# Performance work log

Measured on AMD Instinct MI355X. Metric: run time of the kernel, lower is better.

Reference implementation:

```python
import jax, jax.numpy as jnp
import numpy as np

T, S, B, E, H, F = 100, 4096, 32, 256, 8, 2048
DH = E // H
EPS = 1e-5

def setup_inputs() -> dict:
    key = jax.random.key(0)
    ks = jax.random.split(key, 32)
    n = lambda i, shape, s=1.0: jax.random.normal(ks[i], shape, jnp.float32) * s
    inp = {
        'hidden_states': n(0, (T, B, E)),
        'query_pos': n(1, (T, B, E)),
        'enc_hidden': n(2, (S, B, E)),
        'enc_pos': n(3, (S, B, E)),
        'attn_mask': n(4, (B * H, T, S)),
        # cross-attn (nn.MultiheadAttention) params
        'ca_wq': n(5, (E, E), 0.02), 'ca_bq': jnp.zeros(E),
        'ca_wk': n(6, (E, E), 0.02), 'ca_bk': jnp.zeros(E),
        'ca_wv': n(7, (E, E), 0.02), 'ca_bv': jnp.zeros(E),
        'ca_wo': n(8, (E, E), 0.02), 'ca_bo': jnp.zeros(E),
        # self-attn (Mask2FormerAttention) params
        'sa_wq': n(9, (E, E), 0.02), 'sa_bq': jnp.zeros(E),
        'sa_wk': n(10, (E, E), 0.02), 'sa_bk': jnp.zeros(E),
        'sa_wv': n(11, (E, E), 0.02), 'sa_bv': jnp.zeros(E),
        'sa_wo': n(12, (E, E), 0.02), 'sa_bo': jnp.zeros(E),
        # layer norms
        'ln1_g': jnp.ones(E), 'ln1_b': jnp.zeros(E),
        'ln2_g': jnp.ones(E), 'ln2_b': jnp.zeros(E),
        'ln3_g': jnp.ones(E), 'ln3_b': jnp.zeros(E),
        # FFN
        'fc1_w': n(13, (F, E), 0.02), 'fc1_b': jnp.zeros(F),
        'fc2_w': n(14, (E, F), 0.02), 'fc2_b': jnp.zeros(E),
    }
    return inp

def _ln(x, g, b):
    m = jnp.mean(x, -1, keepdims=True)
    v = jnp.mean(jnp.square(x - m), -1, keepdims=True)
    return (x - m) * jax.lax.rsqrt(v + EPS) * g + b

def _mha(q_in, k_in, v_in, wq, bq, wk, bk, wv, bv, wo, bo, mask):
    # q_in: [B,T,E], k_in/v_in: [B,S,E], mask: [B*H,T,S] additive or None
    b, t, _ = q_in.shape
    s = k_in.shape[1]
    q = (q_in @ wq.T + bq) * (DH ** -0.5)
    k = k_in @ wk.T + bk
    v = v_in @ wv.T + bv
    q = q.reshape(b, t, H, DH).transpose(0, 2, 1, 3)  # [B,H,T,dh]
    k = k.reshape(b, s, H, DH).transpose(0, 2, 1, 3)
    v = v.reshape(b, s, H, DH).transpose(0, 2, 1, 3)
    scores = jnp.einsum('bhtd,bhsd->bhts', q, k)
    if mask is not None:
        scores = scores + mask.reshape(b, H, t, s)
    p = jax.nn.softmax(scores, axis=-1)
    o = jnp.einsum('bhts,bhsd->bhtd', p, v)
    o = o.transpose(0, 2, 1, 3).reshape(b, t, E)
    return o @ wo.T + bo

def reference(hidden_states, query_pos, enc_hidden, enc_pos, attn_mask,
              ca_wq, ca_bq, ca_wk, ca_bk, ca_wv, ca_bv, ca_wo, ca_bo,
              sa_wq, sa_bq, sa_wk, sa_bk, sa_wv, sa_bv, sa_wo, sa_bo,
              ln1_g, ln1_b, ln2_g, ln2_b, ln3_g, ln3_b,
              fc1_w, fc1_b, fc2_w, fc2_b):
    # convert seq-first [T,B,E] -> batch-first [B,T,E]
    hs = hidden_states.transpose(1, 0, 2)
    qp = query_pos.transpose(1, 0, 2)
    enc = enc_hidden.transpose(1, 0, 2)
    ep = enc_pos.transpose(1, 0, 2)
    # masked cross-attention (post-norm), dropout=0
    residual = hs
    x = _mha(hs + qp, enc + ep, enc,
             ca_wq, ca_bq, ca_wk, ca_bk, ca_wv, ca_bv, ca_wo, ca_bo, attn_mask)
    hs = _ln(residual + x, ln1_g, ln1_b)
    # self-attention with query pos embeddings on q and k, no mask
    residual = hs
    x = _mha(hs + qp, hs + qp, hs,
             sa_wq, sa_bq, sa_wk, sa_bk, sa_wv, sa_bv, sa_wo, sa_bo, None)
    hs = _ln(residual + x, ln2_g, ln2_b)
    # FFN
    x = jax.nn.relu(hs @ fc1_w.T + fc1_b) @ fc2_w.T + fc2_b
    hs = _ln(hs + x, ln3_g, ln3_b)
    return hs.transpose(1, 0, 2)  # back to [T,B,E]
```

## Files before the change

### kernel.cpp

```cpp
#include <hip/hip_runtime.h>
#include <hip/hip_bf16.h>
#include <math.h>

#define TQ 100
#define SS 4096
#define BB 32
#define EE 256
#define HH 8
#define FF 2048
#define DHH 32
#define LNEPS 1e-5f

typedef __attribute__((ext_vector_type(8))) short bf16x8;
typedef __attribute__((ext_vector_type(4))) short bf16x4;
typedef __attribute__((ext_vector_type(4))) float f32x4;

__device__ inline unsigned short f2bfu(float f) {
    __hip_bfloat16 h = __float2bfloat16(f);
    return *reinterpret_cast<unsigned short*>(&h);
}

#define PBM 64
#define PBK 32
#define PLDP 40
#define TLP 268

__global__ __launch_bounds__(256)
void cvt_all(const float* s0, const float* s1, const float* s2, const float* s3,
             const float* s4, const float* s5, const float* s6, const float* s7,
             const float* s8, const float* s9,
             unsigned short* d0, unsigned short* d1, unsigned short* d2, unsigned short* d3,
             unsigned short* d4, unsigned short* d5, unsigned short* d6, unsigned short* d7,
             unsigned short* d8, unsigned short* d9)
{
    const int bi = blockIdx.x;
    const float* s; unsigned short* d; int base;
    if (bi < 512) {
        const int seg = bi >> 6;
        base = (bi & 63) * 1024;
        switch (seg) {
            case 0: s = s0; d = d0; break;
            case 1: s = s1; d = d1; break;
            case 2: s = s2; d = d2; break;
            case 3: s = s3; d = d3; break;
            case 4: s = s4; d = d4; break;
            case 5: s = s5; d = d5; break;
            case 6: s = s6; d = d6; break;
            default: s = s7; d = d7; break;
        }
    } else {
        const int r = bi - 512;
        base = (r & 511) * 1024;
        if (r >> 9) { s = s9; d = d9; } else { s = s8; d = d8; }
    }
    const int i = base + threadIdx.x * 4;
    float4 v = *(const float4*)(s + i);
    ushort4 ov;
    ov.x = f2bfu(v.x); ov.y = f2bfu(v.y); ov.z = f2bfu(v.z); ov.w = f2bfu(v.w);
    *(ushort4*)(d + i) = ov;
}

__global__ __launch_bounds__(256)
void proj_kv(const float* __restrict__ enc, const float* __restrict__ ep,
             const __hip_bfloat16* __restrict__ Wk, const float* __restrict__ bk,
             const __hip_bfloat16* __restrict__ Wv, const float* __restrict__ bv,
             __hip_bfloat16* __restrict__ Kout, __hip_bfloat16* __restrict__ Vtout)
{
    __shared__ short Akv[PBM][PLDP];
    __shared__ short Av[PBM][PLDP];
    __shared__ short BkRaw[256 * PLDP];
    __shared__ short BvRaw[256 * PLDP];
    short (*Bk)[PLDP] = (short(*)[PLDP])BkRaw;
    short (*Bv)[PLDP] = (short(*)[PLDP])BvRaw;
    short (*tk)[TLP] = (short(*)[TLP])BkRaw;
    short (*tv)[TLP] = (short(*)[TLP])BvRaw;

    const int tid = threadIdx.x;
    const int m0 = blockIdx.x * PBM;
    const int b = m0 >> 12;
    const int s0 = m0 & (SS - 1);
    const int rr = tid >> 2;
    const int rc = (tid & 3) << 3;
    const long long abase = ((long long)(s0 + rr) * BB + b) * EE + rc;

    const int wv = tid >> 6, l = tid & 63;
    const int wm0 = (wv & 1) * 32, wn0 = (wv >> 1) * 128;
    const int lr16 = l & 15, lk8 = (l >> 4) * 8;

    f32x4 acck[2][8] = {};
    f32x4 accv[2][8] = {};

    for (int k0 = 0; k0 < EE; k0 += PBK) {
        float4 a0 = *(const float4*)(enc + abase + k0);
        float4 a1 = *(const float4*)(enc + abase + k0 + 4);
        float4 e0 = *(const float4*)(ep + abase + k0);
        float4 e1 = *(const float4*)(ep + abase + k0 + 4);
        bf16x8 pv, pkv;
        pv[0] = (short)f2bfu(a0.x); pv[1] = (short)f2bfu(a0.y);
        pv[2] = (short)f2bfu(a0.z); pv[3] = (short)f2bfu(a0.w);
        pv[4] = (short)f2bfu(a1.x); pv[5] = (short)f2bfu(a1.y);
        pv[6] = (short)f2bfu(a1.z); pv[7] = (short)f2bfu(a1.w);
        pkv[0] = (short)f2bfu(a0.x + e0.x); pkv[1] = (short)f2bfu(a0.y + e0.y);
        pkv[2] = (short)f2bfu(a0.z + e0.z); pkv[3] = (short)f2bfu(a0.w + e0.w);
        pkv[4] = (short)f2bfu(a1.x + e1.x); pkv[5] = (short)f2bfu(a1.y + e1.y);
        pkv[6] = (short)f2bfu(a1.z + e1.z); pkv[7] = (short)f2bfu(a1.w + e1.w);

        bf16x8 wkr[4], wvr[4];
        #pragma unroll
        for (int it = 0; it < 4; ++it) {
            wkr[it] = *(const bf16x8*)(Wk + (long long)(rr + it * 64) * EE + k0 + rc);
            wvr[it] = *(const bf16x8*)(Wv + (long long)(rr + it * 64) * EE + k0 + rc);
        }

        __syncthreads();
        *(bf16x8*)&Akv[rr][rc] = pkv;
        *(bf16x8*)&Av[rr][rc]  = pv;
        #pragma unroll
        for (int it = 0; it < 4; ++it) {
            *(bf16x8*)&Bk[rr + it * 64][rc] = wkr[it];
            *(bf16x8*)&Bv[rr + it * 64][rc] = wvr[it];
        }
        __syncthreads();

        bf16x8 ak0 = *(const bf16x8*)&Akv[wm0 + lr16][lk8];
        bf16x8 ak1 = *(const bf16x8*)&Akv[wm0 + 16 + lr16][lk8];
        bf16x8 av0 = *(const bf16x8*)&Av[wm0 + lr16][lk8];
        bf16x8 av1 = *(const bf16x8*)&Av[wm0 + 16 + lr16][lk8];
        #pragma unroll
        for (int j = 0; j < 8; ++j) {
            bf16x8 bk8 = *(const bf16x8*)&Bk[wn0 + j * 16 + lr16][lk8];
            bf16x8 bv8 = *(const bf16x8*)&Bv[wn0 + j * 16 + lr16][lk8];
            acck[0][j] = __builtin_amdgcn_mfma_f32_16x16x32_bf16(ak0, bk8, acck[0][j], 0, 0, 0);
            acck[1][j] = __builtin_amdgcn_mfma_f32_16x16x32_bf16(ak1, bk8, acck[1][j], 0, 0, 0);
            accv[0][j] = __builtin_amdgcn_mfma_f32_16x16x32_bf16(av0, bv8, accv[0][j], 0, 0, 0);
            accv[1][j] = __builtin_amdgcn_mfma_f32_16x16x32_bf16(av1, bv8, accv[1][j], 0, 0, 0);
        }
    }

    const int q4 = (l >> 4) * 4;
    #pragma unroll
    for (int h = 0; h < 2; ++h) {
        __syncthreads();
        if (wm0 == h * 32) {
            #pragma unroll
            for (int i = 0; i < 2; ++i) {
                #pragma unroll
                for (int j = 0; j < 8; ++j) {
                    const int n = wn0 + j * 16 + lr16;
                    const float bik = bk[n], biv = bv[n];
                    #pragma unroll
                    for (int r = 0; r < 4; ++r) {
                        tk[i * 16 + q4 + r][n] = (short)f2bfu(acck[i][j][r] + bik);
                        tv[i * 16 + q4 + r][n] = (short)f2bfu(accv[i][j][r] + biv);
                    }
                }
            }
        }
        __syncthreads();
        #pragma unroll
        for (int it = 0; it < 8; ++it) {
            const int r2 = wv * 8 + it;
            ushort4 v = *(const ushort4*)&tk[r2][l * 4];
            *(ushort4*)(Kout + (long long)(m0 + h * 32 + r2) * EE + l * 4) = v;
        }
        #pragma unroll
        for (int nn = 0; nn < 32; ++nn) {
            const int n = wv * 64 + nn * 2 + (l >> 5);
            const int s = l & 31;
            unsigned short v = (unsigned short)tv[s][n];
            *((unsigned short*)Vtout + (long long)(b * EE + n) * SS + s0 + h * 32 + s) = v;
        }
    }
}

template<int A1G, int A2Q, int A1BF, int OBF, int RELU>
__global__ __launch_bounds__(128)
void mfma_gemm2(const void* __restrict__ A1v, const float* __restrict__ A2,
                const __hip_bfloat16* __restrict__ Wb, const float* __restrict__ bias,
                void* __restrict__ outv, int N, int K, float scale)
{
    __shared__ short As[32][PLDP];
    __shared__ short Bs[128][PLDP];
    const int tid = threadIdx.x;
    const int m0 = blockIdx.x * 32;
    const int n0 = blockIdx.y * 128;
    const int rr = tid >> 2;
    const int rc = (tid & 3) << 3;
    const int row = m0 + rr;

    long long a2row = 0;
    if (A1G || A2Q) {
        int bq = row / TQ, tq = row - bq * TQ;
        a2row = ((long long)(tq * BB + bq)) * EE;
    }
    const long long a1row = A1G ? a2row : (long long)row * K;

    const int wv = tid >> 6, l = tid & 63;
    const int wm0 = wv * 16;
    const int lr16 = l & 15, lk8 = (l >> 4) * 8;

    f32x4 acc[8] = {};

    for (int k0 = 0; k0 < K; k0 += PBK) {
        bf16x8 apack;
        if (A1BF) {
            apack = *(const bf16x8*)((const __hip_bfloat16*)A1v + a1row + k0 + rc);
        } else {
            const float* A1 = (const float*)A1v;
            float4 a0 = *(const float4*)(A1 + a1row + k0 + rc);
            float4 a1 = *(const float4*)(A1 + a1row + k0 + rc + 4);
            if (A2Q) {
                float4 e0 = *(const float4*)(A2 + a2row + k0 + rc);
                float4 e1 = *(const float4*)(A2 + a2row + k0 + rc + 4);
                a0.x += e0.x; a0.y += e0.y; a0.z += e0.z; a0.w += e0.w;
                a1.x += e1.x; a1.y += e1.y; a1.z += e1.z; a1.w += e1.w;
            }
            apack[0] = (short)f2bfu(a0.x); apack[1] = (short)f2bfu(a0.y);
            apack[2] = (short)f2bfu(a0.z); apack[3] = (short)f2bfu(a0.w);
            apack[4] = (short)f2bfu(a1.x); apack[5] = (short)f2bfu(a1.y);
            apack[6] = (short)f2bfu(a1.z); apack[7] = (short)f2bfu(a1.w);
        }

        bf16x8 wreg[4];
        #pragma unroll
        for (int it = 0; it < 4; ++it)
            wreg[it] = *(const bf16x8*)(Wb + (long long)(n0 + rr + it * 32) * K + k0 + rc);

        __syncthreads();
        *(bf16x8*)&As[rr][rc] = apack;
        #pragma unroll
        for (int it = 0; it < 4; ++it)
            *(bf16x8*)&Bs[rr + it * 32][rc] = wreg[it];
        __syncthreads();

        bf16x8 af = *(const bf16x8*)&As[wm0 + lr16][lk8];
        #pragma unroll
        for (int j = 0; j < 8; ++j) {
            bf16x8 bfr = *(const bf16x8*)&Bs[j * 16 + lr16][lk8];
            acc[j] = __builtin_amdgcn_mfma_f32_16x16x32_bf16(af, bfr, acc[j], 0, 0, 0);
        }
    }

    const int q4 = (l >> 4) * 4;
    #pragma unroll
    for (int j = 0; j < 8; ++j) {
        const int n = n0 + j * 16 + lr16;
        const float bi = bias[n];
        #pragma unroll
        for (int r = 0; r < 4; ++r) {
            float v = (acc[j][r] + bi) * scale;
            if (RELU) v = fmaxf(v, 0.f);
            const long long oidx = (long long)(m0 + wm0 + q4 + r) * N + n;
            if (OBF) ((__hip_bfloat16*)outv)[oidx] = __float2bfloat16(v);
            else     ((float*)outv)[oidx] = v;
        }
    }
}

__global__ __launch_bounds__(128)
void qkv_sa(const float* __restrict__ hs1, const float* __restrict__ qp,
            const __hip_bfloat16* __restrict__ Wq, const float* __restrict__ bq,
            const __hip_bfloat16* __restrict__ Wk, const float* __restrict__ bk,
            const __hip_bfloat16* __restrict__ Wv, const float* __restrict__ bv,
            __hip_bfloat16* __restrict__ Qs, __hip_bfloat16* __restrict__ Ks,
            __hip_bfloat16* __restrict__ Vt, int SVT, float qscale)
{
    __shared__ short Aq[32][PLDP];
    __shared__ short Av[32][PLDP];
    __shared__ short Bq[128][PLDP];
    __shared__ short Bk[128][PLDP];
    __shared__ short Bv[128][PLDP];
    const int tid = threadIdx.x;
    const int m0 = blockIdx.x * 32;
    const int n0 = blockIdx.y * 128;
    const int rr = tid >> 2;
    const int rc = (tid & 3) << 3;
    const int row = m0 + rr;
    const int bq_ = row / TQ, tq = row - bq_ * TQ;
    const long long a1row = (long long)row * EE;
    const long long a2row = ((long long)(tq * BB + bq_)) * EE;

    const int wv = tid >> 6, l = tid & 63;
    const int wm0 = wv * 16;
    const int lr16 = l & 15, lk8 = (l >> 4) * 8;

    f32x4 aq[8] = {}, ak[8] = {}, av[8] = {};

    for (int k0 = 0; k0 < EE; k0 += PBK) {
        float4 a0 = *(const float4*)(hs1 + a1row + k0 + rc);
        float4 a1 = *(const float4*)(hs1 + a1row + k0 + rc + 4);
        float4 e0 = *(const float4*)(qp + a2row + k0 + rc);
        float4 e1 = *(const float4*)(qp + a2row + k0 + rc + 4);
        bf16x8 pq, pv;
        pv[0] = (short)f2bfu(a0.x); pv[1] = (short)f2bfu(a0.y);
        pv[2] = (short)f2bfu(a0.z); pv[3] = (short)f2bfu(a0.w);
        pv[4] = (short)f2bfu(a1.x); pv[5] = (short)f2bfu(a1.y);
        pv[6] = (short)f2bfu(a1.z); pv[7] = (short)f2bfu(a1.w);
        pq[0] = (short)f2bfu(a0.x + e0.x); pq[1] = (short)f2bfu(a0.y + e0.y);
        pq[2] = (short)f2bfu(a0.z + e0.z); pq[3] = (short)f2bfu(a0.w + e0.w);
        pq[4] = (short)f2bfu(a1.x + e1.x); pq[5] = (short)f2bfu(a1.y + e1.y);
        pq[6] = (short)f2bfu(a1.z + e1.z); pq[7] = (short)f2bfu(a1.w + e1.w);

        bf16x8 wq8[4], wk8[4], wv8[4];
        #pragma unroll
        for (int it = 0; it < 4; ++it) {
            const long long wr = (long long)(n0 + rr + it * 32) * EE + k0 + rc;
            wq8[it] = *(const bf16x8*)(Wq + wr);
            wk8[it] = *(const bf16x8*)(Wk + wr);
            wv8[it] = *(const bf16x8*)(Wv + wr);
        }

        __syncthreads();
        *(bf16x8*)&Aq[rr][rc] = pq;
        *(bf16x8*)&Av[rr][rc] = pv;
        #pragma unroll
        for (int it = 0; it < 4; ++it) {
            *(bf16x8*)&Bq[rr + it * 32][rc] = wq8[it];
            *(bf16x8*)&Bk[rr + it * 32][rc] = wk8[it];
            *(bf16x8*)&Bv[rr + it * 32][rc] = wv8[it];
        }
        __syncthreads();

        bf16x8 afq = *(const bf16x8*)&Aq[wm0 + lr16][lk8];
        bf16x8 afv = *(const bf16x8*)&Av[wm0 + lr16][lk8];
        #pragma unroll
        for (int j = 0; j < 8; ++j) {
            bf16x8 b1 = *(const bf16x8*)&Bq[j * 16 + lr16][lk8];
            bf16x8 b2 = *(const bf16x8*)&Bk[j * 16 + lr16][lk8];
            bf16x8 b3 = *(const bf16x8*)&Bv[j * 16 + lr16][lk8];
            aq[j] = __builtin_amdgcn_mfma_f32_16x16x32_bf16(afq, b1, aq[j], 0, 0, 0);
            ak[j] = __builtin_amdgcn_mfma_f32_16x16x32_bf16(afq, b2, ak[j], 0, 0, 0);
            av[j] = __builtin_amdgcn_mfma_f32_16x16x32_bf16(afv, b3, av[j], 0, 0, 0);
        }
    }

    const int q4 = (l >> 4) * 4;
    #pragma unroll
    for (int j = 0; j < 8; ++j) {
        const int n = n0 + j * 16 + lr16;
        const float b1 = bq[n], b2 = bk[n], b3 = bv[n];
        #pragma unroll
        for (int r = 0; r < 4; ++r) {
            const int m = m0 + wm0 + q4 + r;
            Qs[(long long)m * EE + n] = __float2bfloat16((aq[j][r] + b1) * qscale);
            Ks[(long long)m * EE + n] = __float2bfloat16(ak[j][r] + b2);
            const int bb = m / TQ, tt = m - bb * TQ;
            Vt[(long long)(bb * EE + n) * SVT + tt] = __float2bfloat16(av[j][r] + b3);
        }
    }
}

#define KVB 32
#define LDP 40

__global__ __launch_bounds__(256, 2)
void flash_mfma(const __hip_bfloat16* __restrict__ Qg,
                const __hip_bfloat16* __restrict__ Kg,
                const __hip_bfloat16* __restrict__ Vtg,
                const float* __restrict__ mask,
                __hip_bfloat16* __restrict__ O,
                int Skv, int SVT)
{
    __shared__ short Ks[2][KVB][LDP];
    __shared__ short Vs[2][KVB][LDP];
    const int tid = threadIdx.x;
    const int l = tid & 63;
    const int g = l >> 4, q16 = l & 15;
    const int chunk = gridDim.x >> 3;
    const int logical = (blockIdx.x & 7) * chunk + (blockIdx.x >> 3);
    const int qb = logical & 1;
    const int bh = logical >> 1;
    const int h = bh & (HH - 1), b = bh >> 3;
    const int q0 = qb * 64 + (tid >> 6) * 16;

    int qc = q0 + q16; if (qc >= TQ) qc = TQ - 1;
    const bf16x8 qfrag = *(const bf16x8*)(Qg + ((long long)(b * TQ + qc)) * EE + h * DHH + g * 8);

    const int srow = tid >> 3;
    const int sseg = (tid & 7) * 4;
    const long long kbase = ((long long)b * Skv) * EE + h * DHH;
    const long long vbase = ((long long)(b * EE + h * DHH)) * SVT;
    const float* mrowp = mask ? mask + ((long long)bh * TQ + qc) * Skv : nullptr;

    f32x4 oacc[2] = {{0.f,0.f,0.f,0.f},{0.f,0.f,0.f,0.f}};
    float mrun = -1e30f, lrun = 0.f;
    const f32x4 zero = {0.f,0.f,0.f,0.f};

    int s_ld = srow; if (s_ld >= Skv) s_ld = Skv - 1;
    bf16x4 kreg = *(const bf16x4*)(Kg + kbase + (long long)s_ld * EE + sseg);
    bf16x4 vreg = *(const bf16x4*)(Vtg + vbase + (long long)srow * SVT + sseg);
    float4 mcur0, mcur1;
    if (mrowp) {
        mcur0 = *(const float4*)(mrowp + g * 4);
        mcur1 = *(const float4*)(mrowp + 16 + g * 4);
    }

    const int nround = (Skv + KVB - 1) / KVB;
    for (int r = 0; r < nround; ++r) {
        const int buf = r & 1;
        *(bf16x4*)&Ks[buf][srow][sseg] = kreg;
        *(bf16x4*)&Vs[buf][srow][sseg] = vreg;
        float4 mnx0, mnx1;
        if (r + 1 < nround) {
            int sn = (r + 1) * KVB + srow; if (sn >= Skv) sn = Skv - 1;
            kreg = *(const bf16x4*)(Kg + kbase + (long long)sn * EE + sseg);
            vreg = *(const bf16x4*)(Vtg + vbase + (long long)srow * SVT + (r + 1) * KVB + sseg);
            if (mrowp) {
                mnx0 = *(const float4*)(mrowp + (r + 1) * KVB + g * 4);
                mnx1 = *(const float4*)(mrowp + (r + 1) * KVB + 16 + g * 4);
            }
        }
        __syncthreads();

        const int s0 = r * KVB;
        f32x4 sT[2];
        #pragma unroll
        for (int t = 0; t < 2; ++t) {
            bf16x8 kf = *(const bf16x8*)&Ks[buf][t * 16 + q16][g * 8];
            sT[t] = __builtin_amdgcn_mfma_f32_16x16x32_bf16(kf, qfrag, zero, 0, 0, 0);
        }
        float sc[8];
        if (mrowp) {
            sc[0] = sT[0][0] + mcur0.x; sc[1] = sT[0][1] + mcur0.y;
            sc[2] = sT[0][2] + mcur0.z; sc[3] = sT[0][3] + mcur0.w;
            sc[4] = sT[1][0] + mcur1.x; sc[5] = sT[1][1] + mcur1.y;
            sc[6] = sT[1][2] + mcur1.z; sc[7] = sT[1][3] + mcur1.w;
        } else {
            #pragma unroll
            for (int t = 0; t < 2; ++t)
                #pragma unroll
                for (int rg = 0; rg < 4; ++rg) {
                    int s = s0 + t * 16 + g * 4 + rg;
                    sc[t*4+rg] = (s < Skv) ? sT[t][rg] : -1e30f;
                }
        }
        float tmax = sc[0];
        #pragma unroll
        for (int i = 1; i < 8; ++i) tmax = fmaxf(tmax, sc[i]);
        tmax = fmaxf(tmax, __shfl_xor(tmax, 16));
        tmax = fmaxf(tmax, __shfl_xor(tmax, 32));
        const float mn = fmaxf(mrun, tmax);
        const float corr = __expf(mrun - mn);
        mrun = mn;
        float ps = 0.f;
        bf16x8 pfrag;
        #pragma unroll
        for (int i = 0; i < 8; ++i) {
            float p = __expf(sc[i] - mn);
            ps += p;
            pfrag[i] = (short)f2bfu(p);
        }
        ps += __shfl_xor(ps, 16);
        ps += __shfl_xor(ps, 32);
        lrun = lrun * corr + ps;
        #pragma unroll
        for (int rg = 0; rg < 4; ++rg) {
            float c = __shfl(corr, g * 4 + rg);
            oacc[0][rg] *= c;
            oacc[1][rg] *= c;
        }
        #pragma unroll
        for (int T = 0; T < 2; ++T) {
            bf16x4 v0 = *(const bf16x4*)&Vs[buf][T * 16 + q16][g * 4];
            bf16x4 v1 = *(const bf16x4*)&Vs[buf][T * 16 + q16][16 + g * 4];
            bf16x8 vf;
            vf[0] = v0[0]; vf[1] = v0[1]; vf[2] = v0[2]; vf[3] = v0[3];
            vf[4] = v1[0]; vf[5] = v1[1]; vf[6] = v1[2]; vf[7] = v1[3];
            oacc[T] = __builtin_amdgcn_mfma_f32_16x16x32_bf16(pfrag, vf, oacc[T], 0, 0, 0);
        }
        mcur0 = mnx0; mcur1 = mnx1;
        __syncthreads();
    }

    float linv[4];
    #pragma unroll
    for (int rg = 0; rg < 4; ++rg)
        linv[rg] = 1.f / __shfl(lrun, g * 4 + rg);
    #pragma unroll
    for (int rg = 0; rg < 4; ++rg) {
        const int q = q0 + g * 4 + rg;
        if (q < TQ) {
            __hip_bfloat16* op = O + ((long long)(b * TQ + q)) * EE + h * DHH + q16;
            op[0]  = __float2bfloat16(oacc[0][rg] * linv[rg]);
            op[16] = __float2bfloat16(oacc[1][rg] * linv[rg]);
        }
    }
}

template<int GATHER_RES, int OUT_T, int OUT_BF>
__global__ __launch_bounds__(256)
void ln_kernel(const float* __restrict__ res, const float* __restrict__ x,
               const float* __restrict__ gam, const float* __restrict__ bet,
               float* __restrict__ out, __hip_bfloat16* __restrict__ outb)
{
    __shared__ float r1[4], r2[4];
    const int m = blockIdx.x;
    const int k = threadIdx.x;
    const int b = m / TQ, t = m - b * TQ;
    const long long roff = GATHER_RES ? ((long long)(t * BB + b)) * EE : (long long)m * EE;
    float v = res[roff + k] + x[(long long)m * EE + k];
    float s = v;
    #pragma unroll
    for (int off = 32; off; off >>= 1) s += __shfl_down(s, off);
    if ((k & 63) == 0) r1[k >> 6] = s;
    __syncthreads();
    const float mu = (r1[0] + r1[1] + r1[2] + r1[3]) * (1.0f / EE);
    const float d = v - mu;
    float s2 = d * d;
    #pragma unroll
    for (int off = 32; off; off >>= 1) s2 += __shfl_down(s2, off);
    if ((k & 63) == 0) r2[k >> 6] = s2;
    __syncthreads();
    const float var = (r2[0] + r2[1] + r2[2] + r2[3]) * (1.0f / EE);
    const float o = d * rsqrtf(var + LNEPS) * gam[k] + bet[k];
    const long long ooff = OUT_T ? ((long long)(t * BB + b)) * EE : (long long)m * EE;
    out[ooff + k] = o;
    if (OUT_BF) outb[(long long)m * EE + k] = __float2bfloat16(o);
}

extern "C" void kernel_launch(void* const* d_in, const int* in_sizes, int n_in,
                              void* d_out, int out_size, void* d_ws, size_t ws_size,
                              hipStream_t stream)
{
    const float* hs    = (const float*)d_in[0];
    const float* qp    = (const float*)d_in[1];
    const float* enc   = (const float*)d_in[2];
    const float* ep    = (const float*)d_in[3];
    const float* mask  = (const float*)d_in[4];
    const float* ca_wq = (const float*)d_in[5];  const float* ca_bq = (const float*)d_in[6];
    const float* ca_wk = (const float*)d_in[7];  const float* ca_bk = (const float*)d_in[8];
    const float* ca_wv = (const float*)d_in[9];  const float* ca_bv = (const float*)d_in[10];
    const float* ca_wo = (const float*)d_in[11]; const float* ca_bo = (const float*)d_in[12];
    const float* sa_wq = (const float*)d_in[13]; const float* sa_bq = (const float*)d_in[14];
    const float* sa_wk = (const float*)d_in[15]; const float* sa_bk = (const float*)d_in[16];
    const float* sa_wv = (const float*)d_in[17]; const float* sa_bv = (const float*)d_in[18];
    const float* sa_wo = (const float*)d_in[19]; const float* sa_bo = (const float*)d_in[20];
    const float* ln1_g = (const float*)d_in[21]; const float* ln1_b = (const float*)d_in[22];
    const float* ln2_g = (const float*)d_in[23]; const float* ln2_b = (const float*)d_in[24];
    const float* ln3_g = (const float*)d_in[25]; const float* ln3_b = (const float*)d_in[26];
    const float* fc1_w = (const float*)d_in[27]; const float* fc1_b = (const float*)d_in[28];
    const float* fc2_w = (const float*)d_in[29]; const float* fc2_b = (const float*)d_in[30];

    const int MQ = BB * TQ;
    const int MK = BB * SS;
    const int SVT2 = 128;

    size_t off = 0;
    char* base = (char*)d_ws;
    auto alloc = [&](size_t bytes) -> void* {
        void* p = base + off; off = (off + bytes + 255) & ~(size_t)255; return p;
    };
    __hip_bfloat16* Kc  = (__hip_bfloat16*)alloc((size_t)MK * EE * 2);
    __hip_bfloat16* Vt  = (__hip_bfloat16*)alloc((size_t)BB * EE * SS * 2);
    __hip_bfloat16* Qc  = (__hip_bfloat16*)alloc((size_t)MQ * EE * 2);
    __hip_bfloat16* Qs  = (__hip_bfloat16*)alloc((size_t)MQ * EE * 2);
    __hip_bfloat16* Ks2 = (__hip_bfloat16*)alloc((size_t)MQ * EE * 2);
    __hip_bfloat16* Vt2 = (__hip_bfloat16*)alloc((size_t)BB * EE * SVT2 * 2);
    __hip_bfloat16* Wq1 = (__hip_bfloat16*)alloc((size_t)EE * EE * 2);
    __hip_bfloat16* Wkb = (__hip_bfloat16*)alloc((size_t)EE * EE * 2);
    __hip_bfloat16* Wvb = (__hip_bfloat16*)alloc((size_t)EE * EE * 2);
    __hip_bfloat16* Wo1 = (__hip_bfloat16*)alloc((size_t)EE * EE * 2);
    __hip_bfloat16* Wq2 = (__hip_bfloat16*)alloc((size_t)EE * EE * 2);
    __hip_bfloat16* Wk2 = (__hip_bfloat16*)alloc((size_t)EE * EE * 2);
    __hip_bfloat16* Wv2 = (__hip_bfloat16*)alloc((size_t)EE * EE * 2);
    __hip_bfloat16* Wo2 = (__hip_bfloat16*)alloc((size_t)EE * EE * 2);
    __hip_bfloat16* Wf1 = (__hip_bfloat16*)alloc((size_t)FF * EE * 2);
    __hip_bfloat16* Wf2 = (__hip_bfloat16*)alloc((size_t)EE * FF * 2);
    __hip_bfloat16* hs2b= (__hip_bfloat16*)alloc((size_t)MQ * EE * 2);
    __hip_bfloat16* h1b = (__hip_bfloat16*)alloc((size_t)MQ * FF * 2);
    __hip_bfloat16* attO  = (__hip_bfloat16*)alloc((size_t)MQ * EE * 2);
    __hip_bfloat16* attO2 = (__hip_bfloat16*)alloc((size_t)MQ * EE * 2);
    float* xproj = (float*)alloc((size_t)MQ * EE * 4);
    float* hs1   = (float*)alloc((size_t)MQ * EE * 4);
    float* xpro2 = (float*)alloc((size_t)MQ * EE * 4);
    float* hs2   = (float*)alloc((size_t)MQ * EE * 4);
    float* xffn  = (float*)alloc((size_t)MQ * EE * 4);

    const float qscale = 0.17677669529663687f;
    dim3 blk(256);

    cvt_all<<<dim3(1536), blk, 0, stream>>>(
        ca_wq, ca_wk, ca_wv, ca_wo, sa_wq, sa_wk, sa_wv, sa_wo, fc1_w, fc2_w,
        (unsigned short*)Wq1, (unsigned short*)Wkb, (unsigned short*)Wvb,
        (unsigned short*)Wo1, (unsigned short*)Wq2, (unsigned short*)Wk2,
        (unsigned short*)Wv2, (unsigned short*)Wo2, (unsigned short*)Wf1,
        (unsigned short*)Wf2);

    mfma_gemm2<1,1,0,1,0><<<dim3(MQ/32, 2), dim3(128), 0, stream>>>(hs, qp, Wq1, ca_bq, Qc, EE, EE, qscale);
    proj_kv<<<dim3(MK/PBM), blk, 0, stream>>>(enc, ep, Wkb, ca_bk, Wvb, ca_bv, Kc, Vt);
    flash_mfma<<<dim3(BB*HH*2), dim3(256), 0, stream>>>(Qc, Kc, Vt, mask, attO, SS, SS);
    mfma_gemm2<0,0,1,0,0><<<dim3(MQ/32, 2), dim3(128), 0, stream>>>(attO, nullptr, Wo1, ca_bo, xproj, EE, EE, 1.f);
    ln_kernel<1,0,0><<<dim3(MQ), blk, 0, stream>>>(hs, xproj, ln1_g, ln1_b, hs1, nullptr);

    qkv_sa<<<dim3(MQ/32, 2), dim3(128), 0, stream>>>(hs1, qp, Wq2, sa_bq, Wk2, sa_bk, Wv2, sa_bv,
                                                     Qs, Ks2, Vt2, SVT2, qscale);
    flash_mfma<<<dim3(BB*HH*2), dim3(256), 0, stream>>>(Qs, Ks2, Vt2, nullptr, attO2, TQ, SVT2);
    mfma_gemm2<0,0,1,0,0><<<dim3(MQ/32, 2), dim3(128), 0, stream>>>(attO2, nullptr, Wo2, sa_bo, xpro2, EE, EE, 1.f);
    ln_kernel<0,0,1><<<dim3(MQ), blk, 0, stream>>>(hs1, xpro2, ln2_g, ln2_b, hs2, hs2b);

    mfma_gemm2<0,0,1,1,1><<<dim3(MQ/32, FF/128), dim3(128), 0, stream>>>(hs2b, nullptr, Wf1, fc1_b, h1b, FF, EE, 1.f);
    mfma_gemm2<0,0,1,0,0><<<dim3(MQ/32, 2), dim3(128), 0, stream>>>(h1b, nullptr, Wf2, fc2_b, xffn, EE, FF, 1.f);
    ln_kernel<0,1,0><<<dim3(MQ), blk, 0, stream>>>(hs2, xffn, ln3_g, ln3_b, (float*)d_out, nullptr);

    (void)in_sizes; (void)n_in; (void)out_size; (void)ws_size;
}
```

Baseline: 432.8 us.

## Split proj_kv K and V GEMMs across 8 waves with prefetched activations

The proj_kv kernel now runs 512 threads per block. Half the waves compute the K projection and half compute the V projection, so each wave holds one accumulator set instead of two. This is meant to lower register pressure and raise occupancy (launch bounds 512,4). The next encoder/pos tile is loaded from global memory right after the LDS barrier so the load overlaps the MFMA work. The store loops are re-split across the 8 waves. The cost is more threads sharing the same LDS tiles and barriers.

After: 378.1 us. 1.14x faster.

```diff
diff --git a/kernel.cpp b/kernel.cpp
--- a/kernel.cpp
+++ b/kernel.cpp
@@ -60,7 +60,7 @@
     *(ushort4*)(d + i) = ov;
 }
 
-__global__ __launch_bounds__(256)
+__global__ __launch_bounds__(512, 4)
 void proj_kv(const float* __restrict__ enc, const float* __restrict__ ep,
              const __hip_bfloat16* __restrict__ Wk, const float* __restrict__ bk,
              const __hip_bfloat16* __restrict__ Wv, const float* __restrict__ bv,
@@ -79,93 +79,92 @@
     const int m0 = blockIdx.x * PBM;
     const int b = m0 >> 12;
     const int s0 = m0 & (SS - 1);
-    const int rr = tid >> 2;
-    const int rc = (tid & 3) << 3;
-    const long long abase = ((long long)(s0 + rr) * BB + b) * EE + rc;
-
-    const int wv = tid >> 6, l = tid & 63;
-    const int wm0 = (wv & 1) * 32, wn0 = (wv >> 1) * 128;
+
+    const int arr = tid >> 3;
+    const int arc = (tid & 7) << 2;
+    const long long abase = ((long long)(s0 + arr) * BB + b) * EE + arc;
+    const int wr = tid >> 1;
+    const int wc = (tid & 1) << 4;
+    const long long wbase = (long long)wr * EE + wc;
+
+    const int w = tid >> 6, l = tid & 63;
+    const int mat = w >> 2;
+    const int wm0 = (w & 1) * 32;
+    const int wn0 = ((w >> 1) & 1) * 128;
     const int lr16 = l & 15, lk8 = (l >> 4) * 8;
 
-    f32x4 acck[2][8] = {};
-    f32x4 accv[2][8] = {};
+    f32x4 acc[2][8] = {};
+
+    float4 a0 = *(const float4*)(enc + abase);
+    float4 e0 = *(const float4*)(ep + abase);
 
     for (int k0 = 0; k0 < EE; k0 += PBK) {
-        float4 a0 = *(const float4*)(enc + abase + k0);
-        float4 a1 = *(const float4*)(enc + abase + k0 + 4);
-        float4 e0 = *(const float4*)(ep + abase + k0);
-        float4 e1 = *(const float4*)(ep + abase + k0 + 4);
-        bf16x8 pv, pkv;
+        bf16x8 wk8a = *(const bf16x8*)(Wk + wbase + k0);
+        bf16x8 wk8b = *(const bf16x8*)(Wk + wbase + k0 + 8);
+        bf16x8 wv8a = *(const bf16x8*)(Wv + wbase + k0);
+        bf16x8 wv8b = *(const bf16x8*)(Wv + wbase + k0 + 8);
+
+        bf16x4 pv, pkv;
         pv[0] = (short)f2bfu(a0.x); pv[1] = (short)f2bfu(a0.y);
         pv[2] = (short)f2bfu(a0.z); pv[3] = (short)f2bfu(a0.w);
-        pv[4] = (short)f2bfu(a1.x); pv[5] = (short)f2bfu(a1.y);
-        pv[6] = (short)f2bfu(a1.z); pv[7] = (short)f2bfu(a1.w);
         pkv[0] = (short)f2bfu(a0.x + e0.x); pkv[1] = (short)f2bfu(a0.y + e0.y);
         pkv[2] = (short)f2bfu(a0.z + e0.z); pkv[3] = (short)f2bfu(a0.w + e0.w);
-        pkv[4] = (short)f2bfu(a1.x + e1.x); pkv[5] = (short)f2bfu(a1.y + e1.y);
-        pkv[6] = (short)f2bfu(a1.z + e1.z); pkv[7] = (short)f2bfu(a1.w + e1.w);
-
-        bf16x8 wkr[4], wvr[4];
-        #pragma unroll
-        for (int it = 0; it < 4; ++it) {
-            wkr[it] = *(const bf16x8*)(Wk + (long long)(rr + it * 64) * EE + k0 + rc);
-            wvr[it] = *(const bf16x8*)(Wv + (long long)(rr + it * 64) * EE + k0 + rc);
-        }
-
-        __syncthreads();
-        *(bf16x8*)&Akv[rr][rc] = pkv;
-        *(bf16x8*)&Av[rr][rc]  = pv;
-        #pragma unroll
-        for (int it = 0; it < 4; ++it) {
-            *(bf16x8*)&Bk[rr + it * 64][rc] = wkr[it];
-            *(bf16x8*)&Bv[rr + it * 64][rc] = wvr[it];
-        }
-        __syncthreads();
-
-        bf16x8 ak0 = *(const bf16x8*)&Akv[wm0 + lr16][lk8];
-        bf16x8 ak1 = *(const bf16x8*)&Akv[wm0 + 16 + lr16][lk8];
-        bf16x8 av0 = *(const bf16x8*)&Av[wm0 + lr16][lk8];
-        bf16x8 av1 = *(const bf16x8*)&Av[wm0 + 16 + lr16][lk8];
+
+        __syncthreads();
+        *(bf16x4*)&Akv[arr][arc] = pkv;
+        *(bf16x4*)&Av[arr][arc]  = pv;
+        *(bf16x8*)&Bk[wr][wc]     = wk8a;
+        *(bf16x8*)&Bk[wr][wc + 8] = wk8b;
+        *(bf16x8*)&Bv[wr][wc]     = wv8a;
+        *(bf16x8*)&Bv[wr][wc + 8] = wv8b;
+        __syncthreads();
+
+        if (k0 + PBK < EE) {
+            a0 = *(const float4*)(enc + abase + k0 + PBK);
+            e0 = *(const float4*)(ep + abase + k0 + PBK);
+        }
+
+        const short (*Am)[PLDP] = mat ? Av : Akv;
+        const short (*Bm)[PLDP] = mat ? Bv : Bk;
+        bf16x8 af0 = *(const bf16x8*)&Am[wm0 + lr16][lk8];
+        bf16x8 af1 = *(const bf16x8*)&Am[wm0 + 16 + lr16][lk8];
         #pragma unroll
         for (int j = 0; j < 8; ++j) {
-            bf16x8 bk8 = *(const bf16x8*)&Bk[wn0 + j * 16 + lr16][lk8];
-            bf16x8 bv8 = *(const bf16x8*)&Bv[wn0 + j * 16 + lr16][lk8];
-            acck[0][j] = __builtin_amdgcn_mfma_f32_16x16x32_bf16(ak0, bk8, acck[0][j], 0, 0, 0);
-            acck[1][j] = __builtin_amdgcn_mfma_f32_16x16x32_bf16(ak1, bk8, acck[1][j], 0, 0, 0);
-            accv[0][j] = __builtin_amdgcn_mfma_f32_16x16x32_bf16(av0, bv8, accv[0][j], 0, 0, 0);
-            accv[1][j] = __builtin_amdgcn_mfma_f32_16x16x32_bf16(av1, bv8, accv[1][j], 0, 0, 0);
-        }
-    }
-
+            bf16x8 b8 = *(const bf16x8*)&Bm[wn0 + j * 16 + lr16][lk8];
+            acc[0][j] = __builtin_amdgcn_mfma_f32_16x16x32_bf16(af0, b8, acc[0][j], 0, 0, 0);
+            acc[1][j] = __builtin_amdgcn_mfma_f32_16x16x32_bf16(af1, b8, acc[1][j], 0, 0, 0);
+        }
+    }
+
+    const float* bias = mat ? bv : bk;
     const int q4 = (l >> 4) * 4;
     #pragma unroll
     for (int h = 0; h < 2; ++h) {
         __syncthreads();
         if (wm0 == h * 32) {
+            short (*tile)[TLP] = mat ? tv : tk;
             #pragma unroll
             for (int i = 0; i < 2; ++i) {
                 #pragma unroll
                 for (int j = 0; j < 8; ++j) {
                     const int n = wn0 + j * 16 + lr16;
-                    const float bik = bk[n], biv = bv[n];
+                    const float bi = bias[n];
                     #pragma unroll
-                    for (int r = 0; r < 4; ++r) {
-                        tk[i * 16 + q4 + r][n] = (short)f2bfu(acck[i][j][r] + bik);
-                        tv[i * 16 + q4 + r][n] = (short)f2bfu(accv[i][j][r] + biv);
-                    }
+                    for (int r = 0; r < 4; ++r)
+                        tile[i * 16 + q4 + r][n] = (short)f2bfu(acc[i][j][r] + bi);
                 }
             }
         }
         __syncthreads();
         #pragma unroll
-        for (int it = 0; it < 8; ++it) {
-            const int r2 = wv * 8 + it;
+        for (int it = 0; it < 4; ++it) {
+            const int r2 = w * 4 + it;
             ushort4 v = *(const ushort4*)&tk[r2][l * 4];
             *(ushort4*)(Kout + (long long)(m0 + h * 32 + r2) * EE + l * 4) = v;
         }
         #pragma unroll
-        for (int nn = 0; nn < 32; ++nn) {
-            const int n = wv * 64 + nn * 2 + (l >> 5);
+        for (int nn = 0; nn < 16; ++nn) {
+            const int n = w * 32 + nn * 2 + (l >> 5);
             const int s = l & 31;
             unsigned short v = (unsigned short)tv[s][n];
             *((unsigned short*)Vtout + (long long)(b * EE + n) * SS + s0 + h * 32 + s) = v;
@@ -587,7 +586,7 @@
         (unsigned short*)Wf2);
 
     mfma_gemm2<1,1,0,1,0><<<dim3(MQ/32, 2), dim3(128), 0, stream>>>(hs, qp, Wq1, ca_bq, Qc, EE, EE, qscale);
-    proj_kv<<<dim3(MK/PBM), blk, 0, stream>>>(enc, ep, Wkb, ca_bk, Wvb, ca_bv, Kc, Vt);
+    proj_kv<<<dim3(MK/PBM), dim3(512), 0, stream>>>(enc, ep, Wkb, ca_bk, Wvb, ca_bv, Kc, Vt);
     flash_mfma<<<dim3(BB*HH*2), dim3(256), 0, stream>>>(Qc, Kc, Vt, mask, attO, SS, SS);
     mfma_gemm2<0,0,1,0,0><<<dim3(MQ/32, 2), dim3(128), 0, stream>>>(attO, nullptr, Wo1, ca_bo, xproj, EE, EE, 1.f);
     ln_kernel<1,0,0><<<dim3(MQ), blk, 0, stream>>>(hs, xproj, ln1_g, ln1_b, hs1, nullptr);
```
